# Kernel tuning notes

Hardware: AMD Instinct MI355X
Metric: run time of the kernel (lower is better)

The kernel has to match this reference:

```python
import jax, jax.numpy as jnp
import numpy as np

B, SL, RATIO = 2, 2048, 16
SG = SL // RATIO          # 128 global tokens
S = SL + SG               # 2176 total sequence
D, H, NC, V = 512, 8, 2, 32000
HD, FF = D // H, 2 * D    # head_dim=64, dim_feedforward=2*d_model
K, R = 4, 4               # rel_pos_max_distance, local_attention_radius
NEG = -1e9


def _ln(x, g, b):
    m = x.mean(-1, keepdims=True)
    v = ((x - m) ** 2).mean(-1, keepdims=True)
    return (x - m) * jax.lax.rsqrt(v + 1e-5) * g + b


def _forward(token_ids, embed, global_token, rel_bias, q_w, q_b, k_w, k_b,
             v_w, v_b, o_w, o_b, ln1_g, ln1_b, ln2_g, ln2_b,
             ff1_w, ff1_b, ff2_w, ff2_b, cls_w1, cls_w2):
    pad = token_ids == 0                                   # B x Sl (padding_idx=0)
    x_long = embed[token_ids]                              # B x Sl x D
    seg_pad = pad.reshape(B, SG, RATIO).all(-1)            # B x Sg: segment fully padded
    x_global = jnp.broadcast_to(global_token, (B, SG, D))  # learned auxiliary global token
    x = jnp.concatenate([x_long, x_global], axis=1)        # B x S x D
    pad_all = jnp.concatenate([pad, seg_pad], axis=1)      # B x S

    # --- global-local attention structure (static masks) ---
    pos = jnp.arange(S)
    is_long = pos < SL
    both_long = is_long[:, None] & is_long[None, :]
    dist = pos[None, :] - pos[:, None]
    # long<->long restricted to local window; any pair involving a global token is allowed
    allowed = jnp.where(both_long, jnp.abs(dist) <= R, True)          # S x S
    rel = jnp.clip(dist, -K, K) + K                                   # S x S in [0, 2K]
    bias = jnp.where(both_long[None], rel_bias[:, rel], 0.0)          # H x S x S

    def heads(t):
        return t.reshape(B, S, H, HD).transpose(0, 2, 1, 3)           # B x H x S x hd
    q = heads(x @ q_w + q_b)
    k = heads(x @ k_w + k_b)
    v = heads(x @ v_w + v_b)
    logits = jnp.einsum('bhid,bhjd->bhij', q, k) / np.float32(np.sqrt(HD)) + bias[None]
    logits = jnp.where(allowed[None, None], logits, NEG)
    logits = jnp.where(pad_all[:, None, None, :], NEG, logits)        # key padding mask
    attn = jax.nn.softmax(logits, axis=-1)
    o = jnp.einsum('bhij,bhjd->bhid', attn, v).transpose(0, 2, 1, 3).reshape(B, S, D)

    # post-norm TransformerEncoderLayer (dropout=0, activation=relu)
    x = _ln(x + (o @ o_w + o_b), ln1_g, ln1_b)
    ff = jax.nn.relu(x @ ff1_w + ff1_b) @ ff2_w + ff2_b
    x = _ln(x + ff, ln2_g, ln2_b)

    # masked mean over global tokens, then MLP head
    zg = x[:, SL:, :]                                                 # B x Sg x D
    zg = jnp.where(seg_pad[..., None], 0.0, zg).sum(1) / (~seg_pad).sum(1, keepdims=True)
    return jax.nn.relu(zg @ cls_w1) @ cls_w2                          # B x Nc


def setup_inputs() -> dict:
    key = jax.random.key(0)
    ks = jax.random.split(key, 16)
    s = 0.02
    embed = jax.random.normal(ks[0], (V, D)) * s
    embed = embed.at[0].set(0.0)  # padding_idx row
    return {
        'x_long_token_ids': jax.random.randint(ks[1], (B, SL), 0, V),
        'embed': embed,
        'global_token': jax.random.normal(ks[2], (D,)) * s,
        'rel_bias': jax.random.normal(ks[3], (H, 2 * K + 1)) * s,
        'q_w': jax.random.normal(ks[4], (D, D)) * s, 'q_b': jnp.zeros((D,)),
        'k_w': jax.random.normal(ks[5], (D, D)) * s, 'k_b': jnp.zeros((D,)),
        'v_w': jax.random.normal(ks[6], (D, D)) * s, 'v_b': jnp.zeros((D,)),
        'o_w': jax.random.normal(ks[7], (D, D)) * s, 'o_b': jnp.zeros((D,)),
        'ln1_g': jnp.ones((D,)), 'ln1_b': jnp.zeros((D,)),
        'ln2_g': jnp.ones((D,)), 'ln2_b': jnp.zeros((D,)),
        'ff1_w': jax.random.normal(ks[8], (D, FF)) * s, 'ff1_b': jnp.zeros((FF,)),
        'ff2_w': jax.random.normal(ks[9], (FF, D)) * s, 'ff2_b': jnp.zeros((D,)),
        'cls_w1': jax.random.normal(ks[10], (D, D // 2)) * s,
        'cls_w2': jax.random.normal(ks[11], (D // 2, NC)) * s,
    }


def reference(x_long_token_ids, embed, global_token, rel_bias, q_w, q_b, k_w, k_b,
              v_w, v_b, o_w, o_b, ln1_g, ln1_b, ln2_g, ln2_b,
              ff1_w, ff1_b, ff2_w, ff2_b, cls_w1, cls_w2):
    return _forward(x_long_token_ids, embed, global_token, rel_bias, q_w, q_b,
                    k_w, k_b, v_w, v_b, o_w, o_b, ln1_g, ln1_b, ln2_g, ln2_b,
                    ff1_w, ff1_b, ff2_w, ff2_b, cls_w1, cls_w2)
```

## Files before the change

kernel.cpp:

```cpp
#include <hip/hip_runtime.h>
#include <hip/hip_bf16.h>
#include <cstddef>

#define B_ 2
#define SL_ 2048
#define RATIO_ 16
#define SG_ 128
#define S_ 2176
#define D_ 512
#define H_ 8
#define HD_ 64
#define FF_ 1024
#define NC_ 2
#define NEG_ (-1.0e9f)
#define MINF_ (-1.0e30f)
#define MROWS_ (B_ * S_)
#define GR_ (B_ * SG_)
#define KC_ 8

typedef __attribute__((ext_vector_type(8))) short short8;
typedef __attribute__((ext_vector_type(4))) float f32x4;

__device__ __forceinline__ void gll16(const void* g, void* l) {
    __builtin_amdgcn_global_load_lds((const __attribute__((address_space(1))) void*)g,
                                     (__attribute__((address_space(3))) void*)l, 16, 0, 0);
}
__device__ __forceinline__ unsigned short f2bf(float x) {
    __hip_bfloat16 h = __float2bfloat16(x);
    return *reinterpret_cast<unsigned short*>(&h);
}
__device__ __forceinline__ float wave_sum(float v) {
#pragma unroll
    for (int off = 1; off < 64; off <<= 1) v += __shfl_xor(v, off);
    return v;
}
#define BARRIER() do { asm volatile("" ::: "memory"); __builtin_amdgcn_s_barrier(); asm volatile("" ::: "memory"); } while (0)

__global__ __launch_bounds__(256) void prep_kernel(const int* __restrict__ ids,
                                                   const float* __restrict__ embed,
                                                   const float* __restrict__ gtok,
                                                   __hip_bfloat16* __restrict__ xb,
                                                   float* __restrict__ xg,
                                                   int* __restrict__ pad_all,
                                                   const float* __restrict__ qw,
                                                   const float* __restrict__ kw,
                                                   const float* __restrict__ vw,
                                                   const float* __restrict__ ow,
                                                   const float* __restrict__ f1w,
                                                   const float* __restrict__ f2w,
                                                   __hip_bfloat16* __restrict__ WqT,
                                                   __hip_bfloat16* __restrict__ WkvT,
                                                   __hip_bfloat16* __restrict__ WoT,
                                                   __hip_bfloat16* __restrict__ W1T,
                                                   __hip_bfloat16* __restrict__ W2T,
                                                   const float* __restrict__ k_b,
                                                   const float* __restrict__ v_b,
                                                   float* __restrict__ kvb) {
    __shared__ float tile[64][65];
    int bid = blockIdx.x, tid = threadIdx.x;
    if (bid < 2176) {
        int half = tid >> 7, lt = tid & 127;
        int row = bid * 2 + half;
        int b = row / S_, s = row % S_;
        const float* src;
        if (s < SL_) {
            int tok = ids[b * SL_ + s];
            src = embed + (size_t)tok * D_;
            if (lt == 0) pad_all[row] = (tok == 0) ? 1 : 0;
        } else {
            src = gtok;
            if (lt == 0) {
                int g = s - SL_;
                int allz = 1;
                for (int r = 0; r < RATIO_; ++r)
                    allz &= (ids[b * SL_ + g * RATIO_ + r] == 0) ? 1 : 0;
                pad_all[row] = allz;
            }
        }
        float4 v = ((const float4*)src)[lt];
        __hip_bfloat16 hb[4] = {__float2bfloat16(v.x), __float2bfloat16(v.y),
                                __float2bfloat16(v.z), __float2bfloat16(v.w)};
        *(uint2*)(xb + (size_t)row * D_ + lt * 4) = *(const uint2*)hb;
        if (s >= SL_)
            ((float4*)(xg + (size_t)(b * SG_ + s - SL_) * D_))[lt] = v;
        return;
    }
    int wbid = bid - 2176;
    if (wbid == 0) {
        for (int i = tid; i < 1024; i += 256)
            kvb[i] = (i < 512) ? k_b[i] : v_b[i - 512];
    }
    const float* W; __hip_bfloat16* Wt; int K, N, tx, ty;
    if (wbid < 192) {
        int which = wbid >> 6, id = wbid & 63;
        W = (which == 0) ? qw : (which == 1) ? kw : vw;
        Wt = (which == 0) ? WqT : (which == 1) ? WkvT : (WkvT + (size_t)512 * 512);
        K = 512; N = 512; tx = id & 7; ty = id >> 3;
    } else if (wbid < 256) {
        int id = wbid - 192; W = ow; Wt = WoT; K = 512; N = 512; tx = id & 7; ty = id >> 3;
    } else if (wbid < 384) {
        int id = wbid - 256; W = f1w; Wt = W1T; K = 512; N = 1024; tx = id & 15; ty = id >> 4;
    } else {
        int id = wbid - 384; W = f2w; Wt = W2T; K = 1024; N = 512; tx = id & 7; ty = id >> 3;
    }
    int n0 = tx * 64, k0 = ty * 64;
    int c = tid & 63, r4 = tid >> 6;
#pragma unroll
    for (int i = 0; i < 16; ++i) {
        int r = i * 4 + r4;
        tile[r][c] = W[(size_t)(k0 + r) * N + n0 + c];
    }
    __syncthreads();
#pragma unroll
    for (int i = 0; i < 16; ++i) {
        int n = i * 4 + r4;
        Wt[(size_t)(n0 + n) * K + k0 + c] = __float2bfloat16(tile[c][n]);
    }
}

__global__ __launch_bounds__(256) void qkv_kernel(const __hip_bfloat16* __restrict__ x_b,
                                                  const __hip_bfloat16* __restrict__ WkvT,
                                                  const float* __restrict__ kvb,
                                                  __hip_bfloat16* __restrict__ kv_bf,
                                                  const __hip_bfloat16* __restrict__ WqT,
                                                  const float* __restrict__ q_b,
                                                  __hip_bfloat16* __restrict__ qg_bf) {
    __shared__ short SA[2][4096];
    __shared__ short SB[2][4096];
    int bid = blockIdx.x, tid = threadIdx.x;
    int w = tid >> 6, lane = tid & 63;
    int wr = w >> 1, wc = w & 1;
    int p0 = tid * 16, rs = p0 >> 6, cs = p0 & 63;

    if (bid < 272) {
        const int K = 512, N = 1024;
        int m0 = (bid >> 3) * 128, n0 = (bid & 7) * 128;
        f32x4 acc[4][4];
#pragma unroll
        for (int m = 0; m < 4; ++m)
#pragma unroll
            for (int n = 0; n < 4; ++n) acc[m][n] = (f32x4){0.f, 0.f, 0.f, 0.f};
        const char* Ab = (const char*)x_b;
        const char* Bb = (const char*)WkvT;
        auto STAGE = [&](int buf, int k0) {
            gll16(Ab + ((size_t)(m0 + rs) * K + k0) * 2 + cs, (char*)SA[buf] + p0);
            gll16(Ab + ((size_t)(m0 + rs + 64) * K + k0) * 2 + cs, (char*)SA[buf] + p0 + 4096);
            gll16(Bb + ((size_t)(n0 + rs) * K + k0) * 2 + cs, (char*)SB[buf] + p0);
            gll16(Bb + ((size_t)(n0 + rs + 64) * K + k0) * 2 + cs, (char*)SB[buf] + p0 + 4096);
        };
        STAGE(0, 0);
        const int nk = K >> 5;
        for (int t = 0; t < nk; ++t) {
            int cur = t & 1;
            if (t + 1 < nk) {
                STAGE(cur ^ 1, (t + 1) << 5);
                asm volatile("s_waitcnt vmcnt(4)" ::: "memory");
            } else {
                asm volatile("s_waitcnt vmcnt(0)" ::: "memory");
            }
            BARRIER();
            short8 af[4], bfr[4];
#pragma unroll
            for (int m = 0; m < 4; ++m)
                af[m] = *(const short8*)&SA[cur][(wr * 64 + m * 16 + (lane & 15)) * 32 + (lane >> 4) * 8];
#pragma unroll
            for (int n = 0; n < 4; ++n)
                bfr[n] = *(const short8*)&SB[cur][(wc * 64 + n * 16 + (lane & 15)) * 32 + (lane >> 4) * 8];
#pragma unroll
            for (int m = 0; m < 4; ++m)
#pragma unroll
                for (int n = 0; n < 4; ++n)
                    acc[m][n] = __builtin_amdgcn_mfma_f32_16x16x32_bf16(af[m], bfr[n], acc[m][n], 0, 0, 0);
            BARRIER();
        }
        int rbase = m0 + wr * 64 + (lane >> 4) * 4;
        int cbase = n0 + wc * 64 + (lane & 15);
#pragma unroll
        for (int m = 0; m < 4; ++m)
#pragma unroll
            for (int n = 0; n < 4; ++n) {
                int col = cbase + n * 16;
                float bv = kvb[col];
#pragma unroll
                for (int j = 0; j < 4; ++j) {
                    int row = rbase + m * 16 + j;
                    kv_bf[(size_t)row * N + col] = __float2bfloat16(acc[m][n][j] + bv);
                }
            }
    } else {
        const int K = 512, N = 512;
        int idx = bid - 272;
        int m0 = (idx >> 3) * 64, n0 = (idx & 7) * 64;
        f32x4 acc[2][2];
#pragma unroll
        for (int m = 0; m < 2; ++m)
#pragma unroll
            for (int n = 0; n < 2; ++n) acc[m][n] = (f32x4){0.f, 0.f, 0.f, 0.f};
        int rl = m0 + rs;
        size_t arow = (size_t)((rl >> 7) * S_ + SL_ + (rl & 127));
        const char* Ab = (const char*)x_b;
        const char* Bb = (const char*)WqT;
        auto STAGE = [&](int buf, int k0) {
            gll16(Ab + (arow * K + k0) * 2 + cs, (char*)SA[buf] + p0);
            gll16(Bb + ((size_t)(n0 + rs) * K + k0) * 2 + cs, (char*)SB[buf] + p0);
        };
        STAGE(0, 0);
        const int nk = K >> 5;
        for (int t = 0; t < nk; ++t) {
            int cur = t & 1;
            if (t + 1 < nk) {
                STAGE(cur ^ 1, (t + 1) << 5);
                asm volatile("s_waitcnt vmcnt(2)" ::: "memory");
            } else {
                asm volatile("s_waitcnt vmcnt(0)" ::: "memory");
            }
            BARRIER();
            short8 af[2], bfr[2];
#pragma unroll
            for (int m = 0; m < 2; ++m)
                af[m] = *(const short8*)&SA[cur][(wr * 32 + m * 16 + (lane & 15)) * 32 + (lane >> 4) * 8];
#pragma unroll
            for (int n = 0; n < 2; ++n)
                bfr[n] = *(const short8*)&SB[cur][(wc * 32 + n * 16 + (lane & 15)) * 32 + (lane >> 4) * 8];
#pragma unroll
            for (int m = 0; m < 2; ++m)
#pragma unroll
                for (int n = 0; n < 2; ++n)
                    acc[m][n] = __builtin_amdgcn_mfma_f32_16x16x32_bf16(af[m], bfr[n], acc[m][n], 0, 0, 0);
            BARRIER();
        }
        int rbase = m0 + wr * 32 + (lane >> 4) * 4;
        int cbase = n0 + wc * 32 + (lane & 15);
#pragma unroll
        for (int m = 0; m < 2; ++m)
#pragma unroll
            for (int n = 0; n < 2; ++n) {
                int col = cbase + n * 16;
                float bv = q_b[col];
#pragma unroll
                for (int j = 0; j < 4; ++j) {
                    int row = rbase + m * 16 + j;
                    qg_bf[(size_t)row * N + col] = __float2bfloat16(acc[m][n][j] + bv);
                }
            }
    }
}

__global__ __launch_bounds__(256) void gemm64_kernel(const __hip_bfloat16* __restrict__ A,
                                                     const __hip_bfloat16* __restrict__ Bt,
                                                     const float* __restrict__ bias,
                                                     const float* __restrict__ Res,
                                                     void* __restrict__ Cout,
                                                     int N, int K, int flags) {
    __shared__ short As[2][64 * 32];
    __shared__ short Bs[2][64 * 32];
    int tid = threadIdx.x;
    int m0 = blockIdx.y * 64, n0 = blockIdx.x * 64;
    int w = tid >> 6, lane = tid & 63;
    int wr = w >> 1, wc = w & 1;

    f32x4 acc[2][2];
#pragma unroll
    for (int m = 0; m < 2; ++m)
#pragma unroll
        for (int n = 0; n < 2; ++n)
            acc[m][n] = (f32x4){0.f, 0.f, 0.f, 0.f};

    int p0 = tid * 16, rs = p0 >> 6, cs = p0 & 63;
    const char* Ab = (const char*)A;
    const char* Bb = (const char*)Bt;

    auto STAGE = [&](int buf, int k0) {
        gll16(Ab + ((size_t)(m0 + rs) * K + k0) * 2 + cs, (char*)As[buf] + p0);
        gll16(Bb + ((size_t)(n0 + rs) * K + k0) * 2 + cs, (char*)Bs[buf] + p0);
    };
    STAGE(0, 0);
    int nk = K >> 5;
    for (int t = 0; t < nk; ++t) {
        int cur = t & 1;
        if (t + 1 < nk) {
            STAGE(cur ^ 1, (t + 1) << 5);
            asm volatile("s_waitcnt vmcnt(2)" ::: "memory");
        } else {
            asm volatile("s_waitcnt vmcnt(0)" ::: "memory");
        }
        BARRIER();
        short8 af[2], bfr[2];
#pragma unroll
        for (int m = 0; m < 2; ++m)
            af[m] = *(const short8*)&As[cur][(wr * 32 + m * 16 + (lane & 15)) * 32 + (lane >> 4) * 8];
#pragma unroll
        for (int n = 0; n < 2; ++n)
            bfr[n] = *(const short8*)&Bs[cur][(wc * 32 + n * 16 + (lane & 15)) * 32 + (lane >> 4) * 8];
#pragma unroll
        for (int m = 0; m < 2; ++m)
#pragma unroll
            for (int n = 0; n < 2; ++n)
                acc[m][n] = __builtin_amdgcn_mfma_f32_16x16x32_bf16(af[m], bfr[n], acc[m][n], 0, 0, 0);
        BARRIER();
    }

    int rbase = m0 + wr * 32 + (lane >> 4) * 4;
    int cbase = n0 + wc * 32 + (lane & 15);
#pragma unroll
    for (int m = 0; m < 2; ++m)
#pragma unroll
        for (int n = 0; n < 2; ++n) {
            int col = cbase + n * 16;
            float bv = bias[col];
#pragma unroll
            for (int j = 0; j < 4; ++j) {
                int row = rbase + m * 16 + j;
                float v = acc[m][n][j] + bv;
                if (flags & 4) v += Res[(size_t)row * N + col];
                if (flags & 1) v = fmaxf(v, 0.0f);
                if (flags & 2)
                    ((__hip_bfloat16*)Cout)[(size_t)row * N + col] = __float2bfloat16(v);
                else
                    ((float*)Cout)[(size_t)row * N + col] = v;
            }
        }
}

#define ATT_LDS_ 28480

__global__ __launch_bounds__(256, 4) void attn_global_kernel(const __hip_bfloat16* __restrict__ Qg,
                                                             const __hip_bfloat16* __restrict__ KV,
                                                             const int* __restrict__ pad_all,
                                                             float* __restrict__ pacc,
                                                             float* __restrict__ pm,
                                                             float* __restrict__ pl) {
    __shared__ __align__(16) char smem[ATT_LDS_];
    short* Qs = (short*)(smem + 0);
    short* Ks = (short*)(smem + 4608);
    short* Vt = (short*)(smem + 13824);
    short* Pl = (short*)(smem + 23040);
    float* padv = (float*)(smem + 27648);
    float* msh  = (float*)(smem + 27968);
    float* lsh  = (float*)(smem + 28224);
    float* Osh  = (float*)smem;

    const int TS[KC_ + 1] = {0, 4, 8, 12, 17, 21, 25, 29, 34};
    int bid = blockIdx.x;
    int c  = bid & 7;
    int qt = (bid >> 3) & 3;
    int h  = (bid >> 5) & 7;
    int b  = bid >> 8;
    int i0c = qt * 32;
    int tid = threadIdx.x;
    int w = tid >> 6, lane = tid & 63;
    int qg = w >> 1, kh = w & 1;
    int cq = lane & 15, g4 = lane >> 4;
    const int* pad = pad_all + b * S_;
    const short* qgp = (const short*)Qg;
    const short* kv  = (const short*)KV;

    {
        int q = tid >> 3, g = tid & 7;
        short8 v = *(const short8*)(qgp + (size_t)(b * SG_ + i0c + q) * D_ + h * HD_ + g * 8);
        *(short8*)(Qs + q * 72 + g * 8) = v;
    }

    float mreg = MINF_, lreg = 0.0f;
    f32x4 ot0 = {0,0,0,0}, ot1 = {0,0,0,0}, ot2 = {0,0,0,0}, ot3 = {0,0,0,0};

    for (int t = TS[c]; t < TS[c + 1]; ++t) {
        int j0 = t * 64;
        __syncthreads();
        {
            int key = tid >> 2, g2 = tid & 3;
            size_t base = (size_t)(b * S_ + j0 + key) * 1024 + h * HD_;
#pragma unroll
            for (int gg = 0; gg < 2; ++gg) {
                int g = g2 + gg * 4;
                short8 kvv = *(const short8*)(kv + base + g * 8);
                *(short8*)(Ks + key * 72 + g * 8) = kvv;
                short8 vv = *(const short8*)(kv + base + 512 + g * 8);
#pragma unroll
                for (int i = 0; i < 8; ++i)
                    Vt[(g * 8 + i) * 72 + key] = vv[i];
            }
            if (tid < 64) padv[tid] = pad[j0 + tid] ? NEG_ : 0.0f;
        }
        __syncthreads();

        short8 qf0 = *(const short8*)(Qs + (qg * 16 + cq) * 72 + 0 + g4 * 8);
        short8 qf1 = *(const short8*)(Qs + (qg * 16 + cq) * 72 + 32 + g4 * 8);
        f32x4 st0 = {0,0,0,0}, st1 = {0,0,0,0};
        {
            short8 kf;
            kf = *(const short8*)(Ks + (kh * 32 + cq) * 72 + 0 + g4 * 8);
            st0 = __builtin_amdgcn_mfma_f32_16x16x32_bf16(kf, qf0, st0, 0, 0, 0);
            kf = *(const short8*)(Ks + (kh * 32 + cq) * 72 + 32 + g4 * 8);
            st0 = __builtin_amdgcn_mfma_f32_16x16x32_bf16(kf, qf1, st0, 0, 0, 0);
            kf = *(const short8*)(Ks + (kh * 32 + 16 + cq) * 72 + 0 + g4 * 8);
            st1 = __builtin_amdgcn_mfma_f32_16x16x32_bf16(kf, qf0, st1, 0, 0, 0);
            kf = *(const short8*)(Ks + (kh * 32 + 16 + cq) * 72 + 32 + g4 * 8);
            st1 = __builtin_amdgcn_mfma_f32_16x16x32_bf16(kf, qf1, st1, 0, 0, 0);
        }
        float sarr[8];
#pragma unroll
        for (int mt = 0; mt < 2; ++mt)
#pragma unroll
            for (int j = 0; j < 4; ++j) {
                int k = kh * 32 + mt * 16 + g4 * 4 + j;
                sarr[mt * 4 + j] = (mt ? st1[j] : st0[j]) * 0.125f + padv[k];
            }
        float cmax = sarr[0];
#pragma unroll
        for (int i = 1; i < 8; ++i) cmax = fmaxf(cmax, sarr[i]);
        cmax = fmaxf(cmax, __shfl_xor(cmax, 16));
        cmax = fmaxf(cmax, __shfl_xor(cmax, 32));
        float mnew = fmaxf(mreg, cmax);
        float fac = __expf(mreg - mnew);
        float parr[8], psum = 0.0f;
#pragma unroll
        for (int i = 0; i < 8; ++i) { parr[i] = __expf(sarr[i] - mnew); psum += parr[i]; }
        psum += __shfl_xor(psum, 16);
        psum += __shfl_xor(psum, 32);
        lreg = lreg * fac + psum;
        mreg = mnew;
        ot0 *= fac; ot1 *= fac; ot2 *= fac; ot3 *= fac;
#pragma unroll
        for (int mt = 0; mt < 2; ++mt) {
            unsigned int lo = (unsigned int)f2bf(parr[mt * 4 + 0]) | ((unsigned int)f2bf(parr[mt * 4 + 1]) << 16);
            unsigned int hi = (unsigned int)f2bf(parr[mt * 4 + 2]) | ((unsigned int)f2bf(parr[mt * 4 + 3]) << 16);
            unsigned int* dst = (unsigned int*)(Pl + (qg * 16 + cq) * 72 + kh * 32 + mt * 16 + g4 * 4);
            dst[0] = lo; dst[1] = hi;
        }
        short8 pf = *(const short8*)(Pl + (qg * 16 + cq) * 72 + kh * 32 + g4 * 8);
        {
            short8 vf;
            vf = *(const short8*)(Vt + (0 * 16 + cq) * 72 + kh * 32 + g4 * 8);
            ot0 = __builtin_amdgcn_mfma_f32_16x16x32_bf16(vf, pf, ot0, 0, 0, 0);
            vf = *(const short8*)(Vt + (1 * 16 + cq) * 72 + kh * 32 + g4 * 8);
            ot1 = __builtin_amdgcn_mfma_f32_16x16x32_bf16(vf, pf, ot1, 0, 0, 0);
            vf = *(const short8*)(Vt + (2 * 16 + cq) * 72 + kh * 32 + g4 * 8);
            ot2 = __builtin_amdgcn_mfma_f32_16x16x32_bf16(vf, pf, ot2, 0, 0, 0);
            vf = *(const short8*)(Vt + (3 * 16 + cq) * 72 + kh * 32 + g4 * 8);
            ot3 = __builtin_amdgcn_mfma_f32_16x16x32_bf16(vf, pf, ot3, 0, 0, 0);
        }
    }

    __syncthreads();
    if (g4 == 0) {
        msh[(qg * 2 + kh) * 16 + cq] = mreg;
        lsh[(qg * 2 + kh) * 16 + cq] = lreg;
    }
    __syncthreads();
    {
        float m0 = msh[(qg * 2 + 0) * 16 + cq], m1 = msh[(qg * 2 + 1) * 16 + cq];
        float Mm = fmaxf(m0, m1);
        float e_self = __expf(mreg - Mm);
        f32x4 o;
        o = ot0 * e_self; *(f32x4*)(Osh + ((qg * 2 + kh) * 16 + cq) * 68 + 0  + g4 * 4) = o;
        o = ot1 * e_self; *(f32x4*)(Osh + ((qg * 2 + kh) * 16 + cq) * 68 + 16 + g4 * 4) = o;
        o = ot2 * e_self; *(f32x4*)(Osh + ((qg * 2 + kh) * 16 + cq) * 68 + 32 + g4 * 4) = o;
        o = ot3 * e_self; *(f32x4*)(Osh + ((qg * 2 + kh) * 16 + cq) * 68 + 48 + g4 * 4) = o;
    }
    __syncthreads();
    {
        int q_all = tid >> 3, d0 = (tid & 7) * 8;
        int qg2 = q_all >> 4, ql = q_all & 15;
        float mm0 = msh[(qg2 * 2 + 0) * 16 + ql], mm1 = msh[(qg2 * 2 + 1) * 16 + ql];
        float MM = fmaxf(mm0, mm1);
        float lt = lsh[(qg2 * 2 + 0) * 16 + ql] * __expf(mm0 - MM) +
                   lsh[(qg2 * 2 + 1) * 16 + ql] * __expf(mm1 - MM);
        int prow = ((c * B_ + b) * H_ + h) * SG_ + qt * 32 + q_all;
#pragma unroll
        for (int i = 0; i < 8; ++i) {
            float a = Osh[((qg2 * 2 + 0) * 16 + ql) * 68 + d0 + i] +
                      Osh[((qg2 * 2 + 1) * 16 + ql) * 68 + d0 + i];
            pacc[(size_t)prow * HD_ + d0 + i] = a;
        }
        if ((tid & 7) == 0) { pm[prow] = MM; pl[prow] = lt; }
    }
}

__global__ __launch_bounds__(256) void attn_combine_kernel(const float* __restrict__ pacc,
                                                           const float* __restrict__ pm,
                                                           const float* __restrict__ pl,
                                                           __hip_bfloat16* __restrict__ Og) {
    int wave = (int)((blockIdx.x * (size_t)blockDim.x + threadIdx.x) >> 6);
    int lane = threadIdx.x & 63;
    int gq = wave & (SG_ - 1);
    int h  = (wave >> 7) & 7;
    int b  = wave >> 10;

    float M = MINF_;
#pragma unroll
    for (int c = 0; c < KC_; ++c) {
        int pidx = ((c * B_ + b) * H_ + h) * SG_ + gq;
        M = fmaxf(M, pm[pidx]);
    }
    float L = 0.0f, Ov = 0.0f;
#pragma unroll
    for (int c = 0; c < KC_; ++c) {
        int pidx = ((c * B_ + b) * H_ + h) * SG_ + gq;
        float e = __expf(pm[pidx] - M);
        L += pl[pidx] * e;
        Ov += pacc[(size_t)pidx * HD_ + lane] * e;
    }
    Og[(size_t)(b * SG_ + gq) * D_ + h * HD_ + lane] = __float2bfloat16(Ov / L);
}

__global__ __launch_bounds__(256) void ln_kernel(const float* __restrict__ A,
                                                 const float* __restrict__ g,
                                                 const float* __restrict__ be,
                                                 float* __restrict__ out,
                                                 __hip_bfloat16* __restrict__ outb,
                                                 int wb) {
    int row = blockIdx.x;
    int tid = threadIdx.x;
    size_t base = (size_t)row * D_;
    float x0 = A[base + tid];
    float x1 = A[base + tid + 256];
    float s1 = x0 + x1;
    float s2 = x0 * x0 + x1 * x1;
    for (int off = 1; off < 64; off <<= 1) {
        s1 += __shfl_xor(s1, off);
        s2 += __shfl_xor(s2, off);
    }
    __shared__ float ws1[4], ws2[4];
    int wid = tid >> 6;
    if ((tid & 63) == 0) { ws1[wid] = s1; ws2[wid] = s2; }
    __syncthreads();
    s1 = ws1[0] + ws1[1] + ws1[2] + ws1[3];
    s2 = ws2[0] + ws2[1] + ws2[2] + ws2[3];
    float mean = s1 * (1.0f / D_);
    float var  = s2 * (1.0f / D_) - mean * mean;
    float rstd = rsqrtf(var + 1e-5f);
    float o0 = (x0 - mean) * rstd * g[tid]       + be[tid];
    float o1 = (x1 - mean) * rstd * g[tid + 256] + be[tid + 256];
    out[base + tid]       = o0;
    out[base + tid + 256] = o1;
    if (wb) {
        outb[base + tid]       = __float2bfloat16(o0);
        outb[base + tid + 256] = __float2bfloat16(o1);
    }
}

__global__ __launch_bounds__(256) void cls_part_kernel(const float* __restrict__ x2g,
                                                       const int* __restrict__ pad_all,
                                                       const float* __restrict__ w1,
                                                       float* __restrict__ part) {
    int kc = blockIdx.x, b = blockIdx.y, tid = threadIdx.x;
    __shared__ float wrow[SG_];
    __shared__ float zpart[4][64];
    __shared__ float zgs[64];
    if (tid < SG_) wrow[tid] = pad_all[b * S_ + SL_ + tid] ? 0.0f : 1.0f;
    __syncthreads();

    int j = tid & 63, grp = tid >> 6;
    float a = 0.0f;
#pragma unroll 8
    for (int g = grp; g < SG_; g += 4)
        a = fmaf(wrow[g], x2g[(size_t)(b * SG_ + g) * D_ + kc * 64 + j], a);
    zpart[grp][j] = a;
    __syncthreads();
    if (tid < 64) {
        float cnt = 0.0f;
#pragma unroll 16
        for (int g = 0; g < SG_; ++g) cnt += wrow[g];
        zgs[tid] = (zpart[0][tid] + zpart[1][tid] + zpart[2][tid] + zpart[3][tid]) / cnt;
    }
    __syncthreads();

    float s = 0.0f;
#pragma unroll 8
    for (int d = 0; d < 64; ++d)
        s = fmaf(zgs[d], w1[(size_t)(kc * 64 + d) * 256 + tid], s);
    part[(b * 8 + kc) * 256 + tid] = s;
}

__global__ __launch_bounds__(256) void cls_fin_kernel(const float* __restrict__ part,
                                                      const float* __restrict__ w2,
                                                      float* __restrict__ out) {
    int b = blockIdx.x, n = threadIdx.x;
    float hsum = 0.0f;
#pragma unroll
    for (int kc = 0; kc < 8; ++kc) hsum += part[(b * 8 + kc) * 256 + n];
    hsum = fmaxf(hsum, 0.0f);
    float o0 = hsum * w2[(size_t)n * NC_ + 0];
    float o1 = hsum * w2[(size_t)n * NC_ + 1];
    o0 = wave_sum(o0);
    o1 = wave_sum(o1);
    __shared__ float r0[4], r1[4];
    if ((n & 63) == 0) { r0[n >> 6] = o0; r1[n >> 6] = o1; }
    __syncthreads();
    if (n == 0) {
        out[b * NC_ + 0] = r0[0] + r0[1] + r0[2] + r0[3];
        out[b * NC_ + 1] = r1[0] + r1[1] + r1[2] + r1[3];
    }
}

extern "C" void kernel_launch(void* const* d_in, const int* in_sizes, int n_in,
                              void* d_out, int out_size, void* d_ws, size_t ws_size,
                              hipStream_t stream) {
    const int*   ids    = (const int*)d_in[0];
    const float* embed  = (const float*)d_in[1];
    const float* gtok   = (const float*)d_in[2];
    const float* q_w    = (const float*)d_in[4];
    const float* q_b    = (const float*)d_in[5];
    const float* k_w    = (const float*)d_in[6];
    const float* k_b    = (const float*)d_in[7];
    const float* v_w    = (const float*)d_in[8];
    const float* v_b    = (const float*)d_in[9];
    const float* o_w    = (const float*)d_in[10];
    const float* o_b    = (const float*)d_in[11];
    const float* ln1_g  = (const float*)d_in[12];
    const float* ln1_b  = (const float*)d_in[13];
    const float* ln2_g  = (const float*)d_in[14];
    const float* ln2_b  = (const float*)d_in[15];
    const float* ff1_w  = (const float*)d_in[16];
    const float* ff1_b  = (const float*)d_in[17];
    const float* ff2_w  = (const float*)d_in[18];
    const float* ff2_b  = (const float*)d_in[19];
    const float* cls_w1 = (const float*)d_in[20];
    const float* cls_w2 = (const float*)d_in[21];

    char* ws = (char*)d_ws;
    __hip_bfloat16* x_b     = (__hip_bfloat16*)(ws + 0);
    __hip_bfloat16* kv_bf   = (__hip_bfloat16*)(ws + 4456448);
    __hip_bfloat16* qg_bf   = (__hip_bfloat16*)(ws + 13369344);
    __hip_bfloat16* og_bf   = (__hip_bfloat16*)(ws + 13631488);
    float*          xg_f32  = (float*)(ws + 13893632);
    float*          tmpA    = (float*)(ws + 14417920);
    float*          x1g     = (float*)(ws + 14942208);
    __hip_bfloat16* x1g_b   = (__hip_bfloat16*)(ws + 15466496);
    __hip_bfloat16* ffh_b   = (__hip_bfloat16*)(ws + 15728640);
    float*          tmpB    = (float*)(ws + 16252928);
    float*          x2g     = (float*)(ws + 16777216);
    __hip_bfloat16* WqT     = (__hip_bfloat16*)(ws + 17301504);
    __hip_bfloat16* WkvT    = (__hip_bfloat16*)(ws + 17825792);
    __hip_bfloat16* WoT     = (__hip_bfloat16*)(ws + 18874368);
    __hip_bfloat16* W1T     = (__hip_bfloat16*)(ws + 19398656);
    __hip_bfloat16* W2T     = (__hip_bfloat16*)(ws + 20447232);
    float*          kvb     = (float*)(ws + 21495808);
    int*            pad_all = (int*)(ws + 21499904);
    float*          pacc    = (float*)(ws + 21520384);
    float*          pm      = (float*)(ws + 25714688);
    float*          pl      = (float*)(ws + 25780224);
    float*          clspart = (float*)(ws + 25845760);

    prep_kernel<<<2688, 256, 0, stream>>>(ids, embed, gtok, x_b, xg_f32, pad_all,
                                          q_w, k_w, v_w, o_w, ff1_w, ff2_w,
                                          WqT, WkvT, WoT, W1T, W2T, k_b, v_b, kvb);

    qkv_kernel<<<304, 256, 0, stream>>>(x_b, WkvT, kvb, kv_bf, WqT, q_b, qg_bf);

    attn_global_kernel<<<512, 256, 0, stream>>>(qg_bf, kv_bf, pad_all, pacc, pm, pl);
    attn_combine_kernel<<<512, 256, 0, stream>>>(pacc, pm, pl, og_bf);

    gemm64_kernel<<<dim3(8, 4), 256, 0, stream>>>(og_bf, WoT, o_b, xg_f32, tmpA, 512, 512, 4);
    ln_kernel<<<GR_, 256, 0, stream>>>(tmpA, ln1_g, ln1_b, x1g, x1g_b, 1);
    gemm64_kernel<<<dim3(16, 4), 256, 0, stream>>>(x1g_b, W1T, ff1_b, nullptr, ffh_b, 1024, 512, 1 | 2);
    gemm64_kernel<<<dim3(8, 4), 256, 0, stream>>>(ffh_b, W2T, ff2_b, x1g, tmpB, 512, 1024, 4);
    ln_kernel<<<GR_, 256, 0, stream>>>(tmpB, ln2_g, ln2_b, x2g, nullptr, 0);

    cls_part_kernel<<<dim3(8, B_), 256, 0, stream>>>(x2g, pad_all, cls_w1, clspart);
    cls_fin_kernel<<<B_, 256, 0, stream>>>(clspart, cls_w2, (float*)d_out);
}
```

Baseline: 87.70 us.

## Fuse attention combine, out-proj, LN1, FFN and LN2 into one tail kernel

```diff
diff --git a/kernel.cpp b/kernel.cpp
--- a/kernel.cpp
+++ b/kernel.cpp
@@ -246,82 +246,6 @@
     }
 }
 
-__global__ __launch_bounds__(256) void gemm64_kernel(const __hip_bfloat16* __restrict__ A,
-                                                     const __hip_bfloat16* __restrict__ Bt,
-                                                     const float* __restrict__ bias,
-                                                     const float* __restrict__ Res,
-                                                     void* __restrict__ Cout,
-                                                     int N, int K, int flags) {
-    __shared__ short As[2][64 * 32];
-    __shared__ short Bs[2][64 * 32];
-    int tid = threadIdx.x;
-    int m0 = blockIdx.y * 64, n0 = blockIdx.x * 64;
-    int w = tid >> 6, lane = tid & 63;
-    int wr = w >> 1, wc = w & 1;
-
-    f32x4 acc[2][2];
-#pragma unroll
-    for (int m = 0; m < 2; ++m)
-#pragma unroll
-        for (int n = 0; n < 2; ++n)
-            acc[m][n] = (f32x4){0.f, 0.f, 0.f, 0.f};
-
-    int p0 = tid * 16, rs = p0 >> 6, cs = p0 & 63;
-    const char* Ab = (const char*)A;
-    const char* Bb = (const char*)Bt;
-
-    auto STAGE = [&](int buf, int k0) {
-        gll16(Ab + ((size_t)(m0 + rs) * K + k0) * 2 + cs, (char*)As[buf] + p0);
-        gll16(Bb + ((size_t)(n0 + rs) * K + k0) * 2 + cs, (char*)Bs[buf] + p0);
-    };
-    STAGE(0, 0);
-    int nk = K >> 5;
-    for (int t = 0; t < nk; ++t) {
-        int cur = t & 1;
-        if (t + 1 < nk) {
-            STAGE(cur ^ 1, (t + 1) << 5);
-            asm volatile("s_waitcnt vmcnt(2)" ::: "memory");
-        } else {
-            asm volatile("s_waitcnt vmcnt(0)" ::: "memory");
-        }
-        BARRIER();
-        short8 af[2], bfr[2];
-#pragma unroll
-        for (int m = 0; m < 2; ++m)
-            af[m] = *(const short8*)&As[cur][(wr * 32 + m * 16 + (lane & 15)) * 32 + (lane >> 4) * 8];
-#pragma unroll
-        for (int n = 0; n < 2; ++n)
-            bfr[n] = *(const short8*)&Bs[cur][(wc * 32 + n * 16 + (lane & 15)) * 32 + (lane >> 4) * 8];
-#pragma unroll
-        for (int m = 0; m < 2; ++m)
-#pragma unroll
-            for (int n = 0; n < 2; ++n)
-                acc[m][n] = __builtin_amdgcn_mfma_f32_16x16x32_bf16(af[m], bfr[n], acc[m][n], 0, 0, 0);
-        BARRIER();
-    }
-
-    int rbase = m0 + wr * 32 + (lane >> 4) * 4;
-    int cbase = n0 + wc * 32 + (lane & 15);
-#pragma unroll
-    for (int m = 0; m < 2; ++m)
-#pragma unroll
-        for (int n = 0; n < 2; ++n) {
-            int col = cbase + n * 16;
-            float bv = bias[col];
-#pragma unroll
-            for (int j = 0; j < 4; ++j) {
-                int row = rbase + m * 16 + j;
-                float v = acc[m][n][j] + bv;
-                if (flags & 4) v += Res[(size_t)row * N + col];
-                if (flags & 1) v = fmaxf(v, 0.0f);
-                if (flags & 2)
-                    ((__hip_bfloat16*)Cout)[(size_t)row * N + col] = __float2bfloat16(v);
-                else
-                    ((float*)Cout)[(size_t)row * N + col] = v;
-            }
-        }
-}
-
 #define ATT_LDS_ 28480
 
 __global__ __launch_bounds__(256, 4) void attn_global_kernel(const __hip_bfloat16* __restrict__ Qg,
@@ -477,66 +401,189 @@
     }
 }
 
-__global__ __launch_bounds__(256) void attn_combine_kernel(const float* __restrict__ pacc,
-                                                           const float* __restrict__ pm,
-                                                           const float* __restrict__ pl,
-                                                           __hip_bfloat16* __restrict__ Og) {
-    int wave = (int)((blockIdx.x * (size_t)blockDim.x + threadIdx.x) >> 6);
-    int lane = threadIdx.x & 63;
-    int gq = wave & (SG_ - 1);
-    int h  = (wave >> 7) & 7;
-    int b  = wave >> 10;
-
-    float M = MINF_;
-#pragma unroll
-    for (int c = 0; c < KC_; ++c) {
-        int pidx = ((c * B_ + b) * H_ + h) * SG_ + gq;
-        M = fmaxf(M, pm[pidx]);
-    }
-    float L = 0.0f, Ov = 0.0f;
-#pragma unroll
-    for (int c = 0; c < KC_; ++c) {
-        int pidx = ((c * B_ + b) * H_ + h) * SG_ + gq;
-        float e = __expf(pm[pidx] - M);
-        L += pl[pidx] * e;
-        Ov += pacc[(size_t)pidx * HD_ + lane] * e;
-    }
-    Og[(size_t)(b * SG_ + gq) * D_ + h * HD_ + lane] = __float2bfloat16(Ov / L);
-}
-
-__global__ __launch_bounds__(256) void ln_kernel(const float* __restrict__ A,
-                                                 const float* __restrict__ g,
-                                                 const float* __restrict__ be,
-                                                 float* __restrict__ out,
-                                                 __hip_bfloat16* __restrict__ outb,
-                                                 int wb) {
-    int row = blockIdx.x;
+__global__ __launch_bounds__(256) void tail_kernel(const float* __restrict__ pacc,
+                                                   const float* __restrict__ pm,
+                                                   const float* __restrict__ pl,
+                                                   const float* __restrict__ xg,
+                                                   const __hip_bfloat16* __restrict__ WoT,
+                                                   const float* __restrict__ o_b,
+                                                   const float* __restrict__ ln1_g,
+                                                   const float* __restrict__ ln1_b,
+                                                   const __hip_bfloat16* __restrict__ W1T,
+                                                   const float* __restrict__ ff1_b,
+                                                   const __hip_bfloat16* __restrict__ W2T,
+                                                   const float* __restrict__ ff2_b,
+                                                   const float* __restrict__ ln2_g,
+                                                   const float* __restrict__ ln2_b,
+                                                   float* __restrict__ x2g) {
+    __shared__ __align__(16) char smem[115968];
+    short* Apan = (short*)smem;
+    short* FFH  = (short*)(smem + 16640);
+    char*  Bst  = smem + 50176;
+    float* Crow = (float*)(smem + 82944);
+
     int tid = threadIdx.x;
-    size_t base = (size_t)row * D_;
-    float x0 = A[base + tid];
-    float x1 = A[base + tid + 256];
-    float s1 = x0 + x1;
-    float s2 = x0 * x0 + x1 * x1;
-    for (int off = 1; off < 64; off <<= 1) {
-        s1 += __shfl_xor(s1, off);
-        s2 += __shfl_xor(s2, off);
-    }
-    __shared__ float ws1[4], ws2[4];
-    int wid = tid >> 6;
-    if ((tid & 63) == 0) { ws1[wid] = s1; ws2[wid] = s2; }
-    __syncthreads();
-    s1 = ws1[0] + ws1[1] + ws1[2] + ws1[3];
-    s2 = ws2[0] + ws2[1] + ws2[2] + ws2[3];
-    float mean = s1 * (1.0f / D_);
-    float var  = s2 * (1.0f / D_) - mean * mean;
-    float rstd = rsqrtf(var + 1e-5f);
-    float o0 = (x0 - mean) * rstd * g[tid]       + be[tid];
-    float o1 = (x1 - mean) * rstd * g[tid + 256] + be[tid + 256];
-    out[base + tid]       = o0;
-    out[base + tid + 256] = o1;
-    if (wb) {
-        outb[base + tid]       = __float2bfloat16(o0);
-        outb[base + tid + 256] = __float2bfloat16(o1);
+    int w = tid >> 6, lane = tid & 63;
+    int r0 = blockIdx.x * 16;
+
+    for (int it = w; it < 128; it += 4) {
+        int r = it >> 3, h = it & 7;
+        int grow = r0 + r;
+        int b = grow >> 7, gq = grow & 127;
+        float M = MINF_;
+#pragma unroll
+        for (int c = 0; c < KC_; ++c)
+            M = fmaxf(M, pm[((c * B_ + b) * H_ + h) * SG_ + gq]);
+        float L = 0.0f, Ov = 0.0f;
+#pragma unroll
+        for (int c = 0; c < KC_; ++c) {
+            int pidx = ((c * B_ + b) * H_ + h) * SG_ + gq;
+            float e = __expf(pm[pidx] - M);
+            L += pl[pidx] * e;
+            Ov += pacc[(size_t)pidx * HD_ + lane] * e;
+        }
+        Apan[r * 520 + h * 64 + lane] = (short)f2bf(Ov / L);
+    }
+    __syncthreads();
+
+    auto GEMM_NT = [&](const short* Ap, int apitch, const __hip_bfloat16* Bt, int K, int n0,
+                       auto&& epi) {
+        f32x4 acc[4];
+#pragma unroll
+        for (int f = 0; f < 4; ++f) acc[f] = (f32x4){0.f, 0.f, 0.f, 0.f};
+        const char* Bb = (const char*)Bt;
+        auto STAGE = [&](int buf, int k0) {
+#pragma unroll
+            for (int p = 0; p < 4; ++p) {
+                int off = p * 4096 + tid * 16;
+                int col = off >> 6, cs2 = off & 63;
+                gll16(Bb + ((size_t)(n0 + col) * K + k0) * 2 + cs2, Bst + buf * 16384 + off);
+            }
+        };
+        STAGE(0, 0);
+        int nk = K >> 5;
+        for (int t = 0; t < nk; ++t) {
+            int cur = t & 1;
+            if (t + 1 < nk) {
+                STAGE(cur ^ 1, (t + 1) << 5);
+                asm volatile("s_waitcnt vmcnt(4)" ::: "memory");
+            } else {
+                asm volatile("s_waitcnt vmcnt(0)" ::: "memory");
+            }
+            BARRIER();
+            short8 af = *(const short8*)&Ap[(lane & 15) * apitch + t * 32 + (lane >> 4) * 8];
+#pragma unroll
+            for (int f = 0; f < 4; ++f) {
+                short8 bf8 = *(const short8*)((short*)Bst + cur * 8192 +
+                                              (w * 64 + f * 16 + (lane & 15)) * 32 + (lane >> 4) * 8);
+                acc[f] = __builtin_amdgcn_mfma_f32_16x16x32_bf16(af, bf8, acc[f], 0, 0, 0);
+            }
+            BARRIER();
+        }
+        epi(acc);
+    };
+
+    for (int n0 = 0; n0 < 512; n0 += 256) {
+        GEMM_NT(Apan, 520, WoT, 512, n0, [&](f32x4* acc) {
+#pragma unroll
+            for (int f = 0; f < 4; ++f) {
+                int col = n0 + w * 64 + f * 16 + (lane & 15);
+                float bv = o_b[col];
+#pragma unroll
+                for (int j = 0; j < 4; ++j) {
+                    int r = (lane >> 4) * 4 + j;
+                    Crow[r * 516 + col] = acc[f][j] + bv + xg[(size_t)(r0 + r) * D_ + col];
+                }
+            }
+        });
+    }
+    __syncthreads();
+
+    {
+#pragma unroll
+        for (int rr = 0; rr < 4; ++rr) {
+            int r = w * 4 + rr;
+            float vv[8], s1 = 0.0f, s2 = 0.0f;
+#pragma unroll
+            for (int i = 0; i < 8; ++i) {
+                float v = Crow[r * 516 + i * 64 + lane];
+                vv[i] = v; s1 += v; s2 += v * v;
+            }
+#pragma unroll
+            for (int off = 1; off < 64; off <<= 1) {
+                s1 += __shfl_xor(s1, off);
+                s2 += __shfl_xor(s2, off);
+            }
+            float mean = s1 * (1.0f / D_);
+            float var  = s2 * (1.0f / D_) - mean * mean;
+            float rstd = rsqrtf(var + 1e-5f);
+#pragma unroll
+            for (int i = 0; i < 8; ++i) {
+                int col = i * 64 + lane;
+                float v = (vv[i] - mean) * rstd * ln1_g[col] + ln1_b[col];
+                Crow[r * 516 + col] = v;
+                Apan[r * 520 + col] = (short)f2bf(v);
+            }
+        }
+    }
+    __syncthreads();
+
+    for (int n0 = 0; n0 < 1024; n0 += 256) {
+        GEMM_NT(Apan, 520, W1T, 512, n0, [&](f32x4* acc) {
+#pragma unroll
+            for (int f = 0; f < 4; ++f) {
+                int col = n0 + w * 64 + f * 16 + (lane & 15);
+                float bv = ff1_b[col];
+#pragma unroll
+                for (int j = 0; j < 4; ++j) {
+                    int r = (lane >> 4) * 4 + j;
+                    FFH[r * 1048 + col] = (short)f2bf(fmaxf(acc[f][j] + bv, 0.0f));
+                }
+            }
+        });
+    }
+    __syncthreads();
+
+    for (int n0 = 0; n0 < 512; n0 += 256) {
+        GEMM_NT(FFH, 1048, W2T, 1024, n0, [&](f32x4* acc) {
+#pragma unroll
+            for (int f = 0; f < 4; ++f) {
+                int col = n0 + w * 64 + f * 16 + (lane & 15);
+                float bv = ff2_b[col];
+#pragma unroll
+                for (int j = 0; j < 4; ++j) {
+                    int r = (lane >> 4) * 4 + j;
+                    Crow[r * 516 + col] = acc[f][j] + bv + Crow[r * 516 + col];
+                }
+            }
+        });
+    }
+    __syncthreads();
+
+    {
+#pragma unroll
+        for (int rr = 0; rr < 4; ++rr) {
+            int r = w * 4 + rr;
+            float vv[8], s1 = 0.0f, s2 = 0.0f;
+#pragma unroll
+            for (int i = 0; i < 8; ++i) {
+                float v = Crow[r * 516 + i * 64 + lane];
+                vv[i] = v; s1 += v; s2 += v * v;
+            }
+#pragma unroll
+            for (int off = 1; off < 64; off <<= 1) {
+                s1 += __shfl_xor(s1, off);
+                s2 += __shfl_xor(s2, off);
+            }
+            float mean = s1 * (1.0f / D_);
+            float var  = s2 * (1.0f / D_) - mean * mean;
+            float rstd = rsqrtf(var + 1e-5f);
+#pragma unroll
+            for (int i = 0; i < 8; ++i) {
+                int col = i * 64 + lane;
+                x2g[(size_t)(r0 + r) * D_ + col] = (vv[i] - mean) * rstd * ln2_g[col] + ln2_b[col];
+            }
+        }
     }
 }
 
@@ -623,13 +670,7 @@
     __hip_bfloat16* x_b     = (__hip_bfloat16*)(ws + 0);
     __hip_bfloat16* kv_bf   = (__hip_bfloat16*)(ws + 4456448);
     __hip_bfloat16* qg_bf   = (__hip_bfloat16*)(ws + 13369344);
-    __hip_bfloat16* og_bf   = (__hip_bfloat16*)(ws + 13631488);
     float*          xg_f32  = (float*)(ws + 13893632);
-    float*          tmpA    = (float*)(ws + 14417920);
-    float*          x1g     = (float*)(ws + 14942208);
-    __hip_bfloat16* x1g_b   = (__hip_bfloat16*)(ws + 15466496);
-    __hip_bfloat16* ffh_b   = (__hip_bfloat16*)(ws + 15728640);
-    float*          tmpB    = (float*)(ws + 16252928);
     float*          x2g     = (float*)(ws + 16777216);
     __hip_bfloat16* WqT     = (__hip_bfloat16*)(ws + 17301504);
     __hip_bfloat16* WkvT    = (__hip_bfloat16*)(ws + 17825792);
@@ -650,13 +691,10 @@
     qkv_kernel<<<304, 256, 0, stream>>>(x_b, WkvT, kvb, kv_bf, WqT, q_b, qg_bf);
 
     attn_global_kernel<<<512, 256, 0, stream>>>(qg_bf, kv_bf, pad_all, pacc, pm, pl);
-    attn_combine_kernel<<<512, 256, 0, stream>>>(pacc, pm, pl, og_bf);
-
-    gemm64_kernel<<<dim3(8, 4), 256, 0, stream>>>(og_bf, WoT, o_b, xg_f32, tmpA, 512, 512, 4);
-    ln_kernel<<<GR_, 256, 0, stream>>>(tmpA, ln1_g, ln1_b, x1g, x1g_b, 1);
-    gemm64_kernel<<<dim3(16, 4), 256, 0, stream>>>(x1g_b, W1T, ff1_b, nullptr, ffh_b, 1024, 512, 1 | 2);
-    gemm64_kernel<<<dim3(8, 4), 256, 0, stream>>>(ffh_b, W2T, ff2_b, x1g, tmpB, 512, 1024, 4);
-    ln_kernel<<<GR_, 256, 0, stream>>>(tmpB, ln2_g, ln2_b, x2g, nullptr, 0);
+
+    tail_kernel<<<16, 256, 0, stream>>>(pacc, pm, pl, xg_f32, WoT, o_b,
+                                        ln1_g, ln1_b, W1T, ff1_b, W2T, ff2_b,
+                                        ln2_g, ln2_b, x2g);
 
     cls_part_kernel<<<dim3(8, B_), 256, 0, stream>>>(x2g, pad_all, cls_w1, clspart);
     cls_fin_kernel<<<B_, 256, 0, stream>>>(clspart, cls_w2, (float*)d_out);
```

Result: slower. 118.3 us (+34.9%).

## Fuse LayerNorm1 into FF1 GEMM and LayerNorm2 into classifier pooling

Applied to the files above, without the earlier changes.

```diff
diff --git a/kernel.cpp b/kernel.cpp
--- a/kernel.cpp
+++ b/kernel.cpp
@@ -504,58 +504,151 @@
     Og[(size_t)(b * SG_ + gq) * D_ + h * HD_ + lane] = __float2bfloat16(Ov / L);
 }
 
-__global__ __launch_bounds__(256) void ln_kernel(const float* __restrict__ A,
-                                                 const float* __restrict__ g,
-                                                 const float* __restrict__ be,
-                                                 float* __restrict__ out,
-                                                 __hip_bfloat16* __restrict__ outb,
-                                                 int wb) {
-    int row = blockIdx.x;
+__global__ __launch_bounds__(256) void ff1_ln_kernel(const float* __restrict__ tmpA,
+                                                     const float* __restrict__ ln1_g,
+                                                     const float* __restrict__ ln1_b,
+                                                     const __hip_bfloat16* __restrict__ W1T,
+                                                     const float* __restrict__ ff1_b,
+                                                     __hip_bfloat16* __restrict__ ffh,
+                                                     float* __restrict__ x1g) {
+    __shared__ __align__(16) short Apan[64 * 520];
+    __shared__ __align__(16) short Bs[2][2048];
     int tid = threadIdx.x;
-    size_t base = (size_t)row * D_;
-    float x0 = A[base + tid];
-    float x1 = A[base + tid + 256];
-    float s1 = x0 + x1;
-    float s2 = x0 * x0 + x1 * x1;
-    for (int off = 1; off < 64; off <<= 1) {
-        s1 += __shfl_xor(s1, off);
-        s2 += __shfl_xor(s2, off);
-    }
-    __shared__ float ws1[4], ws2[4];
-    int wid = tid >> 6;
-    if ((tid & 63) == 0) { ws1[wid] = s1; ws2[wid] = s2; }
-    __syncthreads();
-    s1 = ws1[0] + ws1[1] + ws1[2] + ws1[3];
-    s2 = ws2[0] + ws2[1] + ws2[2] + ws2[3];
-    float mean = s1 * (1.0f / D_);
-    float var  = s2 * (1.0f / D_) - mean * mean;
-    float rstd = rsqrtf(var + 1e-5f);
-    float o0 = (x0 - mean) * rstd * g[tid]       + be[tid];
-    float o1 = (x1 - mean) * rstd * g[tid + 256] + be[tid + 256];
-    out[base + tid]       = o0;
-    out[base + tid + 256] = o1;
-    if (wb) {
-        outb[base + tid]       = __float2bfloat16(o0);
-        outb[base + tid + 256] = __float2bfloat16(o1);
-    }
-}
-
-__global__ __launch_bounds__(256) void cls_part_kernel(const float* __restrict__ x2g,
-                                                       const int* __restrict__ pad_all,
-                                                       const float* __restrict__ w1,
-                                                       float* __restrict__ part) {
+    int w = tid >> 6, lane = tid & 63;
+    int wr = w >> 1, wc = w & 1;
+    int m0 = blockIdx.y * 64, n0 = blockIdx.x * 64;
+    const int K = 512;
+
+#pragma unroll 4
+    for (int rr = 0; rr < 16; ++rr) {
+        int r = w * 16 + rr;
+        size_t base = (size_t)(m0 + r) * D_;
+        float vv[8], s1 = 0.0f, s2 = 0.0f;
+#pragma unroll
+        for (int i = 0; i < 8; ++i) {
+            float v = tmpA[base + i * 64 + lane];
+            vv[i] = v; s1 += v; s2 += v * v;
+        }
+#pragma unroll
+        for (int off = 1; off < 64; off <<= 1) {
+            s1 += __shfl_xor(s1, off);
+            s2 += __shfl_xor(s2, off);
+        }
+        float mean = s1 * (1.0f / D_);
+        float var  = s2 * (1.0f / D_) - mean * mean;
+        float rstd = rsqrtf(var + 1e-5f);
+#pragma unroll
+        for (int i = 0; i < 8; ++i) {
+            int col = i * 64 + lane;
+            float o = (vv[i] - mean) * rstd * ln1_g[col] + ln1_b[col];
+            Apan[r * 520 + col] = (short)f2bf(o);
+            if (blockIdx.x == 0) x1g[base + col] = o;
+        }
+    }
+    __syncthreads();
+
+    f32x4 acc[2][2];
+#pragma unroll
+    for (int m = 0; m < 2; ++m)
+#pragma unroll
+        for (int n = 0; n < 2; ++n)
+            acc[m][n] = (f32x4){0.f, 0.f, 0.f, 0.f};
+    int p0 = tid * 16, rs = p0 >> 6, cs = p0 & 63;
+    const char* Bb = (const char*)W1T;
+    auto STAGE = [&](int buf, int k0) {
+        gll16(Bb + ((size_t)(n0 + rs) * K + k0) * 2 + cs, (char*)Bs[buf] + p0);
+    };
+    STAGE(0, 0);
+    const int nk = K >> 5;
+    for (int t = 0; t < nk; ++t) {
+        int cur = t & 1;
+        if (t + 1 < nk) {
+            STAGE(cur ^ 1, (t + 1) << 5);
+            asm volatile("s_waitcnt vmcnt(1)" ::: "memory");
+        } else {
+            asm volatile("s_waitcnt vmcnt(0)" ::: "memory");
+        }
+        BARRIER();
+        short8 af[2], bfr[2];
+#pragma unroll
+        for (int m = 0; m < 2; ++m)
+            af[m] = *(const short8*)&Apan[(wr * 32 + m * 16 + (lane & 15)) * 520 + t * 32 + (lane >> 4) * 8];
+#pragma unroll
+        for (int n = 0; n < 2; ++n)
+            bfr[n] = *(const short8*)&Bs[cur][(wc * 32 + n * 16 + (lane & 15)) * 32 + (lane >> 4) * 8];
+#pragma unroll
+        for (int m = 0; m < 2; ++m)
+#pragma unroll
+            for (int n = 0; n < 2; ++n)
+                acc[m][n] = __builtin_amdgcn_mfma_f32_16x16x32_bf16(af[m], bfr[n], acc[m][n], 0, 0, 0);
+        BARRIER();
+    }
+
+    int rbase = m0 + wr * 32 + (lane >> 4) * 4;
+    int cbase = n0 + wc * 32 + (lane & 15);
+#pragma unroll
+    for (int m = 0; m < 2; ++m)
+#pragma unroll
+        for (int n = 0; n < 2; ++n) {
+            int col = cbase + n * 16;
+            float bv = ff1_b[col];
+#pragma unroll
+            for (int j = 0; j < 4; ++j) {
+                int row = rbase + m * 16 + j;
+                float v = fmaxf(acc[m][n][j] + bv, 0.0f);
+                ffh[(size_t)row * FF_ + col] = __float2bfloat16(v);
+            }
+        }
+}
+
+__global__ __launch_bounds__(256) void cls_part_ln_kernel(const float* __restrict__ tmpB,
+                                                          const int* __restrict__ pad_all,
+                                                          const float* __restrict__ ln2_g,
+                                                          const float* __restrict__ ln2_b,
+                                                          const float* __restrict__ w1,
+                                                          float* __restrict__ part) {
     int kc = blockIdx.x, b = blockIdx.y, tid = threadIdx.x;
+    int w = tid >> 6, lane = tid & 63;
     __shared__ float wrow[SG_];
+    __shared__ float rmean[SG_], rrstd[SG_];
+    __shared__ float g2s[64], b2s[64];
     __shared__ float zpart[4][64];
     __shared__ float zgs[64];
     if (tid < SG_) wrow[tid] = pad_all[b * S_ + SL_ + tid] ? 0.0f : 1.0f;
+    if (tid >= 128 && tid < 192) { g2s[tid - 128] = ln2_g[kc * 64 + tid - 128]; }
+    if (tid >= 192) { b2s[tid - 192] = ln2_b[kc * 64 + tid - 192]; }
+
+    for (int rr = 0; rr < 32; ++rr) {
+        int r = w * 32 + rr;
+        size_t base = (size_t)(b * SG_ + r) * D_;
+        float s1 = 0.0f, s2 = 0.0f;
+#pragma unroll
+        for (int i = 0; i < 8; ++i) {
+            float v = tmpB[base + i * 64 + lane];
+            s1 += v; s2 += v * v;
+        }
+#pragma unroll
+        for (int off = 1; off < 64; off <<= 1) {
+            s1 += __shfl_xor(s1, off);
+            s2 += __shfl_xor(s2, off);
+        }
+        if (lane == 0) {
+            float mean = s1 * (1.0f / D_);
+            float var  = s2 * (1.0f / D_) - mean * mean;
+            rmean[r] = mean;
+            rrstd[r] = rsqrtf(var + 1e-5f);
+        }
+    }
     __syncthreads();
 
     int j = tid & 63, grp = tid >> 6;
     float a = 0.0f;
 #pragma unroll 8
-    for (int g = grp; g < SG_; g += 4)
-        a = fmaf(wrow[g], x2g[(size_t)(b * SG_ + g) * D_ + kc * 64 + j], a);
+    for (int g = grp; g < SG_; g += 4) {
+        float v = tmpB[(size_t)(b * SG_ + g) * D_ + kc * 64 + j];
+        v = (v - rmean[g]) * rrstd[g] * g2s[j] + b2s[j];
+        a = fmaf(wrow[g], v, a);
+    }
     zpart[grp][j] = a;
     __syncthreads();
     if (tid < 64) {
@@ -627,10 +720,8 @@
     float*          xg_f32  = (float*)(ws + 13893632);
     float*          tmpA    = (float*)(ws + 14417920);
     float*          x1g     = (float*)(ws + 14942208);
-    __hip_bfloat16* x1g_b   = (__hip_bfloat16*)(ws + 15466496);
     __hip_bfloat16* ffh_b   = (__hip_bfloat16*)(ws + 15728640);
     float*          tmpB    = (float*)(ws + 16252928);
-    float*          x2g     = (float*)(ws + 16777216);
     __hip_bfloat16* WqT     = (__hip_bfloat16*)(ws + 17301504);
     __hip_bfloat16* WkvT    = (__hip_bfloat16*)(ws + 17825792);
     __hip_bfloat16* WoT     = (__hip_bfloat16*)(ws + 18874368);
@@ -653,11 +744,9 @@
     attn_combine_kernel<<<512, 256, 0, stream>>>(pacc, pm, pl, og_bf);
 
     gemm64_kernel<<<dim3(8, 4), 256, 0, stream>>>(og_bf, WoT, o_b, xg_f32, tmpA, 512, 512, 4);
-    ln_kernel<<<GR_, 256, 0, stream>>>(tmpA, ln1_g, ln1_b, x1g, x1g_b, 1);
-    gemm64_kernel<<<dim3(16, 4), 256, 0, stream>>>(x1g_b, W1T, ff1_b, nullptr, ffh_b, 1024, 512, 1 | 2);
+    ff1_ln_kernel<<<dim3(16, 4), 256, 0, stream>>>(tmpA, ln1_g, ln1_b, W1T, ff1_b, ffh_b, x1g);
     gemm64_kernel<<<dim3(8, 4), 256, 0, stream>>>(ffh_b, W2T, ff2_b, x1g, tmpB, 512, 1024, 4);
-    ln_kernel<<<GR_, 256, 0, stream>>>(tmpB, ln2_g, ln2_b, x2g, nullptr, 0);
-
-    cls_part_kernel<<<dim3(8, B_), 256, 0, stream>>>(x2g, pad_all, cls_w1, clspart);
+
+    cls_part_ln_kernel<<<dim3(8, B_), 256, 0, stream>>>(tmpB, pad_all, ln2_g, ln2_b, cls_w1, clspart);
     cls_fin_kernel<<<B_, 256, 0, stream>>>(clspart, cls_w2, (float*)d_out);
 }
```

Result: slower. 108.4 us (+23.6%).
